# Kernel optimization log

Hardware: AMD Instinct MI355X
Metric: run time of the kernel (lower is better)

Reference implementation:

```python
import jax, jax.numpy as jnp
import numpy as np

B, H, W, DIM = 8, 64, 64, 256
HEADS, DH = 8, 64
HID = HEADS * DH  # 512
EPS = 1e-5


def setup_inputs() -> dict:
    key = jax.random.key(0)
    k0, k1, k2 = jax.random.split(key, 3)
    return {
        "x": jax.random.normal(k0, (B, H, W, DIM), dtype=jnp.float32),
        "w_qkv": jax.random.normal(k1, (DIM, 3 * HID), dtype=jnp.float32) / np.sqrt(DIM),
        "gn_scale": jnp.ones((HID,), jnp.float32),
        "gn_bias": jnp.zeros((HID,), jnp.float32),
        "w_out": jax.random.normal(k2, (HID, DIM), dtype=jnp.float32) / np.sqrt(HID),
        "b_out": jnp.zeros((DIM,), jnp.float32),
    }


def reference(x, w_qkv, gn_scale, gn_bias, w_out, b_out):
    b, h, w, c = x.shape
    n = h * w
    scale = DH ** -0.5
    # 1x1 conv (no bias) == channel matmul
    qkv = jnp.einsum('bxyc,cf->bxyf', x, w_qkv)
    q, k, v = jnp.split(qkv, 3, axis=-1)
    # 'b x y (h c) -> b h c (x y)'
    to_heads = lambda t: t.reshape(b, n, HEADS, DH).transpose(0, 2, 3, 1)
    q, k, v = map(to_heads, (q, k, v))  # [b, heads, d, n]
    q = jax.nn.softmax(q, axis=-2) * scale  # softmax over feature dim d
    k = jax.nn.softmax(k, axis=-1)          # softmax over token dim n
    context = jnp.einsum('bhdn,bhen->bhde', k, v)   # small d x e context
    out = jnp.einsum('bhde,bhdn->bhen', context, q)  # [b, heads, e, n]
    # 'b h c (x y) -> b x y (h c)'
    out = out.transpose(0, 3, 1, 2).reshape(b, h, w, HID)
    # GroupNorm with 1 group: normalize over (H, W, C) per sample
    mu = out.mean(axis=(1, 2, 3), keepdims=True)
    var = out.var(axis=(1, 2, 3), keepdims=True)
    out = (out - mu) * jax.lax.rsqrt(var + EPS) * gn_scale + gn_bias
    # final 1x1 conv with bias
    return jnp.einsum('bxyf,fc->bxyc', out, w_out) + b_out
```

## Files before the change

kernel.cpp:

```cpp
#include <hip/hip_runtime.h>


typedef unsigned short ushort_t;
typedef __attribute__((ext_vector_type(8))) short short8;
typedef __attribute__((ext_vector_type(4))) float floatx4;

__device__ __forceinline__ ushort_t f2b(float f) {
  unsigned int i;
  __builtin_memcpy(&i, &f, 4);
  unsigned int r = (i + 0x7FFFu + ((i >> 16) & 1u)) >> 16;
  return (ushort_t)r;
}

__device__ __forceinline__ void load_lds16(const ushort_t* g, ushort_t* l) {
  __builtin_amdgcn_global_load_lds(
      (const __attribute__((address_space(1))) unsigned int*)g,
      (__attribute__((address_space(3))) unsigned int*)l, 16, 0, 0);
}

__global__ __launch_bounds__(256) void prep_all(
    const float* __restrict__ x, const float* __restrict__ w_qkv,
    const float* __restrict__ gn_scale, const float* __restrict__ gn_bias,
    const float* __restrict__ w_out, const float* __restrict__ b_out,
    ushort_t* __restrict__ xb, ushort_t* __restrict__ wqkvT,
    ushort_t* __restrict__ w2T, float* __restrict__ gw1,
    float* __restrict__ bias2) {
  __shared__ ushort_t t[32][33];
  int bid = blockIdx.x;
  if (bid < 8192) {
    long i = ((long)bid * 256 + threadIdx.x) * 4;
    float4 v = *(const float4*)(x + i);
    ushort4 o;
    o.x = f2b(v.x);
    o.y = f2b(v.y);
    o.z = f2b(v.z);
    o.w = f2b(v.w);
    *(ushort4*)(xb + i) = o;
    return;
  }
  bid -= 8192;
  if (bid < 384) {
    int c0 = (bid % 48) * 32, r0 = (bid / 48) * 32;
    int tx = threadIdx.x & 31, ty = threadIdx.x >> 5;
    for (int i = 0; i < 32; i += 8)
      t[ty + i][tx] = f2b(w_qkv[(long)(r0 + ty + i) * 1536 + c0 + tx]);
    __syncthreads();
    for (int i = 0; i < 32; i += 8)
      wqkvT[(long)(c0 + ty + i) * 256 + r0 + tx] = t[tx][ty + i];
    return;
  }
  bid -= 384;
  if (bid < 128) {
    int c0 = (bid % 8) * 32, r0 = (bid / 8) * 32;
    int tx = threadIdx.x & 31, ty = threadIdx.x >> 5;
    for (int i = 0; i < 32; i += 8) {
      float s = gn_scale[r0 + ty + i];
      t[ty + i][tx] = f2b(w_out[(long)(r0 + ty + i) * 256 + c0 + tx] * s);
    }
    __syncthreads();
    for (int i = 0; i < 32; i += 8)
      w2T[(long)(c0 + ty + i) * 512 + r0 + tx] = t[tx][ty + i];
    return;
  }
  int c = threadIdx.x;
  float g1 = 0.f, b2 = 0.f;
  for (int f = 0; f < 512; ++f) {
    float w = w_out[f * 256 + c];
    g1 += gn_scale[f] * w;
    b2 += gn_bias[f] * w;
  }
  gw1[c] = g1;
  bias2[c] = b2 + b_out[c];
}

__global__ __launch_bounds__(256, 4) void kvctx_kernel(
    const ushort_t* __restrict__ xb, const ushort_t* __restrict__ wqkvT,
    float* __restrict__ ctxP, float* __restrict__ ksumP) {
  __shared__ __align__(16) char lds[32768];
  ushort_t* kTs = (ushort_t*)lds;
  ushort_t* vTs = (ushort_t*)(lds + 16384);

  int gid = blockIdx.x;
  int h = gid >> 8;
  int c0i = gid & 255;
  int b = c0i >> 5;
  int cy = c0i & 31;
  int bh = b * 8 + h;
  int tid = threadIdx.x, wv = tid >> 6, lane = tid & 63;
  int wm = wv & 1, wfk = wv >> 1;
  int l15 = lane & 15, quad = lane >> 4;
  long m0 = (long)b * 4096 + cy * 128;

  floatx4 zero = {0.f, 0.f, 0.f, 0.f};
  floatx4 acc[4][4];
  for (int i = 0; i < 4; i++)
    for (int j = 0; j < 4; j++) acc[i][j] = zero;

  auto stage = [&](int p, int k0) {
    ushort_t* Ab = (ushort_t*)(lds + p * 16384);
    ushort_t* Bb = Ab + 4096;
#pragma unroll
    for (int r = 0; r < 2; ++r) {
      int chunk = r * 256 + tid;
      int row = chunk >> 2, kc = chunk & 3;
      int gc = kc ^ (row & 3);
      long arow = (row < 64 ? 512 : 960) + h * 64 + row;
      load_lds16(wqkvT + arow * 256 + k0 + gc * 8, Ab + chunk * 8);
      load_lds16(xb + (m0 + row) * 256 + k0 + gc * 8, Bb + chunk * 8);
    }
  };

  stage(0, 0);
  __syncthreads();
#pragma unroll
  for (int t = 0; t < 8; ++t) {
    int p = t & 1;
    if (t < 7) stage(p ^ 1, (t + 1) * 32);
    ushort_t* Ab = (ushort_t*)(lds + p * 16384);
    ushort_t* Bb = Ab + 4096;
    short8 af[4], bfr[4];
#pragma unroll
    for (int mt = 0; mt < 4; mt++) {
      int row = wfk * 64 + mt * 16 + l15;
      int slot = quad ^ (row & 3);
      af[mt] = *(const short8*)(Ab + row * 32 + slot * 8);
    }
#pragma unroll
    for (int ft = 0; ft < 4; ft++) {
      int rowb = wm * 64 + ft * 16 + l15;
      int slot = quad ^ (rowb & 3);
      bfr[ft] = *(const short8*)(Bb + rowb * 32 + slot * 8);
    }
#pragma unroll
    for (int mt = 0; mt < 4; mt++)
#pragma unroll
      for (int ft = 0; ft < 4; ft++)
        acc[mt][ft] = __builtin_amdgcn_mfma_f32_16x16x32_bf16(
            af[mt], bfr[ft], acc[mt][ft], 0, 0, 0);
    __syncthreads();
  }

  {
    ushort_t* T = wfk ? vTs : kTs;
#pragma unroll
    for (int mt = 0; mt < 4; mt++)
#pragma unroll
      for (int ft = 0; ft < 4; ft++) {
        int n = wm * 64 + ft * 16 + l15;
        int c = n >> 3, u = n & 7;
#pragma unroll
        for (int r = 0; r < 4; r++) {
          int d = mt * 16 + quad * 4 + r;
          float v = acc[mt][ft][r];
          if (!wfk) v = __expf(v);
          int slot = (c & 8) | ((c ^ d) & 7);
          T[d * 128 + slot * 8 + u] = f2b(v);
        }
      }
  }
  __syncthreads();

  floatx4 cacc[4], acc1;
  for (int i = 0; i < 4; i++) cacc[i] = zero;
  acc1 = zero;
  short8 ones;
#pragma unroll
  for (int u = 0; u < 8; ++u) ones[u] = (short)0x3F80;
#pragma unroll
  for (int ks = 0; ks < 4; ++ks) {
    int d = wv * 16 + l15;
    int cidx = ks * 4 + quad;
    int sa = (cidx & 8) | ((cidx ^ d) & 7);
    short8 a = *(const short8*)(kTs + d * 128 + sa * 8);
    short8 bf[4];
#pragma unroll
    for (int ft = 0; ft < 4; ++ft) {
      int e = ft * 16 + l15;
      int sb = (cidx & 8) | ((cidx ^ e) & 7);
      bf[ft] = *(const short8*)(vTs + e * 128 + sb * 8);
    }
#pragma unroll
    for (int ft = 0; ft < 4; ++ft)
      cacc[ft] = __builtin_amdgcn_mfma_f32_16x16x32_bf16(a, bf[ft], cacc[ft],
                                                         0, 0, 0);
    acc1 = __builtin_amdgcn_mfma_f32_16x16x32_bf16(a, ones, acc1, 0, 0, 0);
  }
  float* cb = ctxP + ((long)cy * 64 + bh) * 4096;
#pragma unroll
  for (int ft = 0; ft < 4; ++ft)
    *(floatx4*)&cb[(ft * 16 + l15) * 64 + wv * 16 + quad * 4] = cacc[ft];
  if (l15 == 0) {
    float* kb = ksumP + ((long)cy * 64 + bh) * 64;
    *(floatx4*)&kb[wv * 16 + quad * 4] = acc1;
  }
}

__global__ __launch_bounds__(256) void reduce_kernel(
    const float* __restrict__ ctxP, const float* __restrict__ ksumP,
    ushort_t* __restrict__ ctxB) {
  int bid = blockIdx.x;
  int bh = bid >> 4;
  int j = (bid & 15) * 256 + threadIdx.x;
  int e = j >> 6, d = j & 63;
  float ks = 0.f;
#pragma unroll
  for (int c = 0; c < 32; ++c) ks += ksumP[((long)c * 64 + bh) * 64 + d];
  float s = 0.f;
#pragma unroll
  for (int c = 0; c < 32; ++c) s += ctxP[((long)c * 64 + bh) * 4096 + j];
  int slot = (d >> 3) ^ (e & 7);
  ctxB[(long)bh * 4096 + e * 64 + slot * 8 + (d & 7)] = f2b(s / ks);
}

__global__ __launch_bounds__(256, 4) void qattn_kernel(
    const ushort_t* __restrict__ xb, const ushort_t* __restrict__ wqT,
    const ushort_t* __restrict__ ctxB, ushort_t* __restrict__ A2,
    float* __restrict__ gstats) {
  __shared__ __align__(16) char lds[32800];
  ushort_t* P = (ushort_t*)lds;
  ushort_t* Od = (ushort_t*)lds;
  float* red = (float*)(lds + 32768);

  int tid = threadIdx.x;
  int bx = blockIdx.x, by = blockIdx.y;
  long m0 = (long)bx * 128;
  long f0 = (long)by * 128;
  int wv = tid >> 6, lane = tid & 63;
  int wm = wv & 1, wf = wv >> 1;
  int l15 = lane & 15, quad = lane >> 4;
  int b = bx >> 5;

  floatx4 acc[4][4];
  floatx4 zero = {0.f, 0.f, 0.f, 0.f};
  for (int i = 0; i < 4; i++)
    for (int j = 0; j < 4; j++) acc[i][j] = zero;

  auto stage = [&](int p, int k0) {
    ushort_t* Ab = (ushort_t*)(lds + p * 16384);
    ushort_t* Bb = Ab + 4096;
#pragma unroll
    for (int r = 0; r < 2; ++r) {
      int chunk = r * 256 + tid;
      int row = chunk >> 2, kc = chunk & 3;
      int gc = kc ^ (row & 3);
      load_lds16(xb + (m0 + row) * 256 + k0 + gc * 8, Ab + chunk * 8);
      load_lds16(wqT + (f0 + row) * 256 + k0 + gc * 8, Bb + chunk * 8);
    }
  };

  stage(0, 0);
  __syncthreads();
#pragma unroll
  for (int t = 0; t < 8; ++t) {
    int p = t & 1;
    if (t < 7) stage(p ^ 1, (t + 1) * 32);
    ushort_t* Ab = (ushort_t*)(lds + p * 16384);
    ushort_t* Bb = Ab + 4096;
    short8 af[4], bfr[4];
#pragma unroll
    for (int mt = 0; mt < 4; mt++) {
      int row = wm * 64 + mt * 16 + l15;
      int slot = quad ^ (row & 3);
      af[mt] = *(const short8*)(Ab + row * 32 + slot * 8);
    }
#pragma unroll
    for (int ft = 0; ft < 4; ft++) {
      int rowb = wf * 64 + ft * 16 + l15;
      int slot = quad ^ (rowb & 3);
      bfr[ft] = *(const short8*)(Bb + rowb * 32 + slot * 8);
    }
#pragma unroll
    for (int mt = 0; mt < 4; mt++)
#pragma unroll
      for (int ft = 0; ft < 4; ft++)
        acc[mt][ft] = __builtin_amdgcn_mfma_f32_16x16x32_bf16(
            af[mt], bfr[ft], acc[mt][ft], 0, 0, 0);
    __syncthreads();
  }

  const ushort_t* cg = ctxB + ((long)(b * 8 + by * 2 + wf)) * 4096;
  short8 cfr0[4];
#pragma unroll
  for (int ft = 0; ft < 4; ++ft) {
    int e = ft * 16 + l15;
    int slot = quad ^ (e & 7);
    cfr0[ft] = *(const short8*)(cg + e * 64 + slot * 8);
  }

  float rs[4][4];
#pragma unroll
  for (int mt = 0; mt < 4; mt++)
#pragma unroll
    for (int r = 0; r < 4; r++) rs[mt][r] = 0.f;
#pragma unroll
  for (int mt = 0; mt < 4; mt++)
#pragma unroll
    for (int ft = 0; ft < 4; ft++)
#pragma unroll
      for (int r = 0; r < 4; r++) {
        float e = __expf(acc[mt][ft][r]);
        acc[mt][ft][r] = e;
        rs[mt][r] += e;
      }
#pragma unroll
  for (int mt = 0; mt < 4; mt++)
#pragma unroll
    for (int r = 0; r < 4; r++) {
      float t = rs[mt][r];
      t += __shfl_xor(t, 1);
      t += __shfl_xor(t, 2);
      t += __shfl_xor(t, 4);
      t += __shfl_xor(t, 8);
      rs[mt][r] = 0.125f / t;
    }

  {
    ushort_t* Pw = P + wf * 8192;
#pragma unroll
    for (int mt = 0; mt < 4; mt++)
#pragma unroll
      for (int ft = 0; ft < 4; ft++) {
        int d = ft * 16 + l15;
#pragma unroll
        for (int r = 0; r < 4; r++) {
          int row = wm * 64 + mt * 16 + quad * 4 + r;
          int slot = (d >> 3) ^ (row & 7);
          Pw[row * 64 + slot * 8 + (d & 7)] = f2b(acc[mt][ft][r] * rs[mt][r]);
        }
      }
  }

  short8 cfr1[4];
#pragma unroll
  for (int ft = 0; ft < 4; ++ft) {
    int e = ft * 16 + l15;
    int slot = (4 + quad) ^ (e & 7);
    cfr1[ft] = *(const short8*)(cg + e * 64 + slot * 8);
  }

  floatx4 o[4][4];
  for (int i = 0; i < 4; i++)
    for (int j = 0; j < 4; j++) o[i][j] = zero;
  {
    const ushort_t* Pr = P + wf * 8192;
    short8 af[4];
#pragma unroll
    for (int mt = 0; mt < 4; mt++) {
      int row = wm * 64 + mt * 16 + l15;
      int slot = quad ^ (row & 7);
      af[mt] = *(const short8*)(Pr + row * 64 + slot * 8);
    }
#pragma unroll
    for (int mt = 0; mt < 4; mt++)
#pragma unroll
      for (int ft = 0; ft < 4; ft++)
        o[mt][ft] = __builtin_amdgcn_mfma_f32_16x16x32_bf16(af[mt], cfr0[ft],
                                                            o[mt][ft], 0, 0,
                                                            0);
#pragma unroll
    for (int mt = 0; mt < 4; mt++) {
      int row = wm * 64 + mt * 16 + l15;
      int slot = (4 + quad) ^ (row & 7);
      af[mt] = *(const short8*)(Pr + row * 64 + slot * 8);
    }
#pragma unroll
    for (int mt = 0; mt < 4; mt++)
#pragma unroll
      for (int ft = 0; ft < 4; ft++)
        o[mt][ft] = __builtin_amdgcn_mfma_f32_16x16x32_bf16(af[mt], cfr1[ft],
                                                            o[mt][ft], 0, 0,
                                                            0);
  }

  float lsum = 0.f, lss = 0.f;
#pragma unroll
  for (int mt = 0; mt < 4; mt++)
#pragma unroll
    for (int ft = 0; ft < 4; ft++)
#pragma unroll
      for (int r = 0; r < 4; r++) {
        float v = o[mt][ft][r];
        lsum += v;
        lss += v * v;
      }

  __syncthreads();

#pragma unroll
  for (int mt = 0; mt < 4; mt++)
#pragma unroll
    for (int ft = 0; ft < 4; ft++) {
      int cl = wf * 64 + ft * 16 + l15;
      int c = cl >> 3, u = cl & 7;
#pragma unroll
      for (int r = 0; r < 4; r++) {
        int rl = wm * 64 + mt * 16 + quad * 4 + r;
        int slot = (c & 8) | ((c ^ rl) & 7);
        Od[rl * 128 + slot * 8 + u] = f2b(o[mt][ft][r]);
      }
    }
  __syncthreads();

  {
    ushort_t* a2g = A2 + ((long)bx * 4 + by) * 16384;
#pragma unroll
    for (int s = 0; s < 8; ++s) {
      int off = s * 2048 + tid * 8;
      int row = off >> 7;
      int c2 = (off & 127) >> 3;
      int slot = (c2 & 8) | ((c2 ^ row) & 7);
      *(short8*)(a2g + off) = *(const short8*)(Od + row * 128 + slot * 8);
    }
  }

  for (int s = 32; s > 0; s >>= 1) {
    lsum += __shfl_xor(lsum, s);
    lss += __shfl_xor(lss, s);
  }
  if (lane == 0) {
    red[wv * 2] = lsum;
    red[wv * 2 + 1] = lss;
  }
  __syncthreads();
  if (tid == 0) {
    float a = 0.f, c = 0.f;
    for (int w2 = 0; w2 < 4; w2++) {
      a += red[w2 * 2];
      c += red[w2 * 2 + 1];
    }
    atomicAdd(&gstats[b * 2], a);
    atomicAdd(&gstats[b * 2 + 1], c);
  }
}

__global__ __launch_bounds__(256, 4) void gemm_out(
    const ushort_t* __restrict__ A, const ushort_t* __restrict__ Bt,
    float* __restrict__ C, const float* __restrict__ gstats,
    const float* __restrict__ gw1, const float* __restrict__ bias2) {
  __shared__ __align__(16) char lds[24576];
  int tid = threadIdx.x;
  int bxc = blockIdx.x;
  int byr = blockIdx.y;
  long m0 = (long)byr * 64;
  long f0 = (long)bxc * 128;
  int wv = tid >> 6, lane = tid & 63;
  int wm = wv & 1, wf = wv >> 1;
  int l15 = lane & 15, quad = lane >> 4;

  floatx4 acc[2][4];
  floatx4 zero = {0.f, 0.f, 0.f, 0.f};
  for (int i = 0; i < 2; i++)
    for (int j = 0; j < 4; j++) acc[i][j] = zero;

  auto stage = [&](int p, int k0) {
    ushort_t* Ab = (ushort_t*)(lds + p * 12288);
    ushort_t* Bb = Ab + 2048;
    const ushort_t* At = A + ((long)(byr >> 1) * 4 + (k0 >> 7)) * 16384 +
                         (long)(byr & 1) * 64 * 128 + (k0 & 127);
    {
      int row = tid >> 2, kc = tid & 3;
      int gc = kc ^ (row & 3);
      load_lds16(At + row * 128 + gc * 8, Ab + tid * 8);
    }
#pragma unroll
    for (int r = 0; r < 2; ++r) {
      int chunk = r * 256 + tid;
      int row = chunk >> 2, kc = chunk & 3;
      int gc = kc ^ (row & 3);
      load_lds16(Bt + (f0 + row) * 512 + k0 + gc * 8, Bb + chunk * 8);
    }
  };

  stage(0, 0);
  __syncthreads();
  for (int t = 0; t < 16; ++t) {
    int p = t & 1;
    if (t < 15) stage(p ^ 1, (t + 1) * 32);
    ushort_t* Ab = (ushort_t*)(lds + p * 12288);
    ushort_t* Bb = Ab + 2048;
    short8 af[2], bfr[4];
#pragma unroll
    for (int mt = 0; mt < 2; mt++) {
      int row = wm * 32 + mt * 16 + l15;
      int slot = quad ^ (row & 3);
      af[mt] = *(const short8*)(Ab + row * 32 + slot * 8);
    }
#pragma unroll
    for (int ft = 0; ft < 4; ft++) {
      int rowb = wf * 64 + ft * 16 + l15;
      int slot = quad ^ (rowb & 3);
      bfr[ft] = *(const short8*)(Bb + rowb * 32 + slot * 8);
    }
#pragma unroll
    for (int mt = 0; mt < 2; mt++)
#pragma unroll
      for (int ft = 0; ft < 4; ft++)
        acc[mt][ft] = __builtin_amdgcn_mfma_f32_16x16x32_bf16(
            af[mt], bfr[ft], acc[mt][ft], 0, 0, 0);
    __syncthreads();
  }

  int b = (int)(m0 >> 12);
  float cnt = 4096.f * 512.f;
  float mu = gstats[b * 2] / cnt;
  float var = gstats[b * 2 + 1] / cnt - mu * mu;
  float rsv = rsqrtf(var + 1e-5f);
#pragma unroll
  for (int mt = 0; mt < 2; mt++)
#pragma unroll
    for (int ft = 0; ft < 4; ft++) {
      long col = f0 + wf * 64 + ft * 16 + l15;
      float c1 = bias2[col] - rsv * mu * gw1[col];
#pragma unroll
      for (int r = 0; r < 4; r++) {
        long row = m0 + wm * 32 + mt * 16 + quad * 4 + r;
        C[row * 256 + col] = rsv * acc[mt][ft][r] + c1;
      }
    }
}

extern "C" void kernel_launch(void* const* d_in, const int* in_sizes, int n_in,
                              void* d_out, int out_size, void* d_ws,
                              size_t ws_size, hipStream_t stream) {
  const float* x = (const float*)d_in[0];
  const float* w_qkv = (const float*)d_in[1];
  const float* gn_scale = (const float*)d_in[2];
  const float* gn_bias = (const float*)d_in[3];
  const float* w_out = (const float*)d_in[4];
  const float* b_out = (const float*)d_in[5];
  float* out = (float*)d_out;

  char* w = (char*)d_ws;
  ushort_t* xb = (ushort_t*)(w + 0);
  ushort_t* A2 = (ushort_t*)(w + 16777216);
  float* ctxP = (float*)(w + 50331648);
  float* ksumP = (float*)(w + 83886080);
  ushort_t* wqkvT = (ushort_t*)(w + 84410368);
  ushort_t* w2T = (ushort_t*)(w + 85196800);
  ushort_t* ctxB = (ushort_t*)(w + 85458944);
  float* gstats = (float*)(w + 85983232);
  float* bias2 = (float*)(w + 85983360);
  float* gw1 = (float*)(w + 85984384);

  hipMemsetAsync(gstats, 0, 64, stream);

  prep_all<<<8705, 256, 0, stream>>>(x, w_qkv, gn_scale, gn_bias, w_out,
                                     b_out, xb, wqkvT, w2T, gw1, bias2);
  kvctx_kernel<<<2048, 256, 0, stream>>>(xb, wqkvT, ctxP, ksumP);
  reduce_kernel<<<1024, 256, 0, stream>>>(ctxP, ksumP, ctxB);
  qattn_kernel<<<dim3(256, 4), 256, 0, stream>>>(xb, wqkvT, ctxB, A2, gstats);
  gemm_out<<<dim3(2, 512), 256, 0, stream>>>(A2, w2T, out, gstats, gw1,
                                             bias2);
}
```

Baseline: 221.0 us.

## Fuse context reduction into kvctx kernel via last-block atomic counter

```diff
diff --git a/kernel.cpp b/kernel.cpp
--- a/kernel.cpp
+++ b/kernel.cpp
@@ -75,8 +75,10 @@
 
 __global__ __launch_bounds__(256, 4) void kvctx_kernel(
     const ushort_t* __restrict__ xb, const ushort_t* __restrict__ wqkvT,
-    float* __restrict__ ctxP, float* __restrict__ ksumP) {
+    float* __restrict__ ctxP, float* __restrict__ ksumP,
+    ushort_t* __restrict__ ctxB, unsigned int* __restrict__ done) {
   __shared__ __align__(16) char lds[32768];
+  __shared__ int sh_last;
   ushort_t* kTs = (ushort_t*)lds;
   ushort_t* vTs = (ushort_t*)(lds + 16384);
 
@@ -193,23 +195,38 @@
     float* kb = ksumP + ((long)cy * 64 + bh) * 64;
     *(floatx4*)&kb[wv * 16 + quad * 4] = acc1;
   }
-}
-
-__global__ __launch_bounds__(256) void reduce_kernel(
-    const float* __restrict__ ctxP, const float* __restrict__ ksumP,
-    ushort_t* __restrict__ ctxB) {
-  int bid = blockIdx.x;
-  int bh = bid >> 4;
-  int j = (bid & 15) * 256 + threadIdx.x;
-  int e = j >> 6, d = j & 63;
-  float ks = 0.f;
-#pragma unroll
-  for (int c = 0; c < 32; ++c) ks += ksumP[((long)c * 64 + bh) * 64 + d];
-  float s = 0.f;
-#pragma unroll
-  for (int c = 0; c < 32; ++c) s += ctxP[((long)c * 64 + bh) * 4096 + j];
-  int slot = (d >> 3) ^ (e & 7);
-  ctxB[(long)bh * 4096 + e * 64 + slot * 8 + (d & 7)] = f2b(s / ks);
+
+  __threadfence();
+  if (tid == 0) sh_last = (atomicAdd(&done[bh], 1u) == 31u);
+  __syncthreads();
+  if (!sh_last) return;
+  __threadfence();
+
+  float* ksLds = (float*)lds;
+  if (tid < 64) {
+    float ks = 0.f;
+#pragma unroll
+    for (int c = 0; c < 32; ++c) ks += ksumP[((long)c * 64 + bh) * 64 + tid];
+    ksLds[tid] = 1.0f / ks;
+  }
+  __syncthreads();
+
+  int j0 = tid * 16;
+#pragma unroll
+  for (int q4 = 0; q4 < 4; ++q4) {
+    floatx4 s = zero;
+#pragma unroll
+    for (int c = 0; c < 32; ++c)
+      s = s + *(const floatx4*)&ctxP[((long)c * 64 + bh) * 4096 + j0 + q4 * 4];
+#pragma unroll
+    for (int k = 0; k < 4; ++k) {
+      int j = j0 + q4 * 4 + k;
+      int e = j >> 6, d = j & 63;
+      int slot = (d >> 3) ^ (e & 7);
+      ctxB[(long)bh * 4096 + e * 64 + slot * 8 + (d & 7)] =
+          f2b(s[k] * ksLds[d]);
+    }
+  }
 }
 
 __global__ __launch_bounds__(256, 4) void qattn_kernel(
@@ -539,15 +556,15 @@
   ushort_t* w2T = (ushort_t*)(w + 85196800);
   ushort_t* ctxB = (ushort_t*)(w + 85458944);
   float* gstats = (float*)(w + 85983232);
-  float* bias2 = (float*)(w + 85983360);
-  float* gw1 = (float*)(w + 85984384);
-
-  hipMemsetAsync(gstats, 0, 64, stream);
+  unsigned int* done = (unsigned int*)(w + 85983296);
+  float* bias2 = (float*)(w + 85983616);
+  float* gw1 = (float*)(w + 85984640);
+
+  hipMemsetAsync(gstats, 0, 320, stream);
 
   prep_all<<<8705, 256, 0, stream>>>(x, w_qkv, gn_scale, gn_bias, w_out,
                                      b_out, xb, wqkvT, w2T, gw1, bias2);
-  kvctx_kernel<<<2048, 256, 0, stream>>>(xb, wqkvT, ctxP, ksumP);
-  reduce_kernel<<<1024, 256, 0, stream>>>(ctxP, ksumP, ctxB);
+  kvctx_kernel<<<2048, 256, 0, stream>>>(xb, wqkvT, ctxP, ksumP, ctxB, done);
   qattn_kernel<<<dim3(256, 4), 256, 0, stream>>>(xb, wqkvT, ctxB, A2, gstats);
   gemm_out<<<dim3(2, 512), 256, 0, stream>>>(A2, w2T, out, gstats, gw1,
                                              bias2);
```

Measured after the change: 565.8 us. 2.56x slower.
